# Kernel tuning notes

Hardware: AMD Instinct MI355X
Metric: run time of the kernel (lower is better)

## Reference

```python
import jax, jax.numpy as jnp
import numpy as np

B, S, LD, Hh, Ww = 64, 32, 16, 32, 18
D, NH, HD, FF, L = 512, 8, 64, 2048, 6
IN = LD * Hh * Ww  # 9216
EPS = 1e-5


def setup_inputs() -> dict:
    key = jax.random.key(0)
    ks = jax.random.split(key, 8)
    p = lambda k, s: jax.random.normal(k, s, jnp.float32) * 0.02
    return {
        "x": jax.random.normal(ks[0], (B, S, LD, Hh, Ww), jnp.float32),
        "inp_w": p(ks[1], (D, IN)), "inp_b": jnp.zeros((D,), jnp.float32),
        "in_proj_w": p(ks[2], (L, 3 * D, D)), "in_proj_b": jnp.zeros((L, 3 * D), jnp.float32),
        "out_w": p(ks[3], (L, D, D)), "out_b": jnp.zeros((L, D), jnp.float32),
        "ln1_w": jnp.ones((L, D), jnp.float32), "ln1_b": jnp.zeros((L, D), jnp.float32),
        "ln2_w": jnp.ones((L, D), jnp.float32), "ln2_b": jnp.zeros((L, D), jnp.float32),
        "ff1_w": p(ks[4], (L, FF, D)), "ff1_b": jnp.zeros((L, FF), jnp.float32),
        "ff2_w": p(ks[5], (L, D, FF)), "ff2_b": jnp.zeros((L, D), jnp.float32),
        "outp_w": p(ks[6], (IN, D)), "outp_b": jnp.zeros((IN,), jnp.float32),
    }


def _layernorm(x, w, b):
    mu = jnp.mean(x, -1, keepdims=True)
    var = jnp.mean(jnp.square(x - mu), -1, keepdims=True)
    return (x - mu) * jax.lax.rsqrt(var + EPS) * w + b


def _rope(x, cos, sin):
    # x: [B,S,NH,HD]; torchtune interleaved-pair rotation, rope applied BEFORE qk projection
    x2 = x.reshape(*x.shape[:-1], HD // 2, 2)
    x0, x1 = x2[..., 0], x2[..., 1]
    c = cos[None, :, None, :]
    s = sin[None, :, None, :]
    out = jnp.stack([x0 * c - x1 * s, x1 * c + x0 * s], axis=-1)
    return out.reshape(x.shape)


def reference(x, inp_w, inp_b, in_proj_w, in_proj_b, out_w, out_b,
              ln1_w, ln1_b, ln2_w, ln2_b, ff1_w, ff1_b, ff2_w, ff2_b,
              outp_w, outp_b):
    b, s = x.shape[0], x.shape[1]
    h = x.reshape(b, s, IN) @ inp_w.T + inp_b  # [B,S,D]

    theta = 1.0 / (10000.0 ** (jnp.arange(0, HD, 2, dtype=jnp.float32) / HD))
    ang = jnp.arange(s, dtype=jnp.float32)[:, None] * theta  # [S, HD/2]
    cos, sin = jnp.cos(ang), jnp.sin(ang)
    mask = jnp.triu(jnp.full((s, s), -jnp.inf, jnp.float32), k=1)  # causal additive mask
    scale = 1.0 / np.sqrt(HD)

    for i in range(L):
        # RoPE on full hidden state (pre-projection), used for q and k; v uses unrotated h
        hr = _rope(h.reshape(b, s, NH, HD), cos, sin).reshape(b, s, D)
        wq, wk, wv = in_proj_w[i, :D], in_proj_w[i, D:2 * D], in_proj_w[i, 2 * D:]
        bq, bk, bv = in_proj_b[i, :D], in_proj_b[i, D:2 * D], in_proj_b[i, 2 * D:]
        q = (hr @ wq.T + bq).reshape(b, s, NH, HD)
        k = (hr @ wk.T + bk).reshape(b, s, NH, HD)
        v = (h @ wv.T + bv).reshape(b, s, NH, HD)
        scores = jnp.einsum('bqhd,bkhd->bhqk', q, k) * scale + mask
        attn = jax.nn.softmax(scores, axis=-1)
        ctx = jnp.einsum('bhqk,bkhd->bqhd', attn, v).reshape(b, s, D)
        sa = ctx @ out_w[i].T + out_b[i]
        h = _layernorm(h + sa, ln1_w[i], ln1_b[i])  # post-norm (norm_first=False)
        ff = jax.nn.gelu(h @ ff1_w[i].T + ff1_b[i], approximate=False) @ ff2_w[i].T + ff2_b[i]
        h = _layernorm(h + ff, ln2_w[i], ln2_b[i])

    out = h @ outp_w.T + outp_b
    return out.reshape(b, s, LD, Hh, Ww)
```

## Files before the change

kernel.cpp:

```cpp
#include <hip/hip_runtime.h>
#include <hip/hip_bf16.h>
#include <math.h>


typedef __attribute__((ext_vector_type(8))) short bf16x8;
typedef __attribute__((ext_vector_type(4))) short bf16x4;
typedef __attribute__((ext_vector_type(8))) float f32x8;
typedef __attribute__((ext_vector_type(4))) float f32x4;

#define LN_EPS 1e-5f

__device__ inline float bf2f(__hip_bfloat16 v) { return __bfloat162float(v); }
__device__ inline __hip_bfloat16 f2bf(float f) { return __float2bfloat16(f); }

__device__ __forceinline__ void gload_lds16(const __hip_bfloat16* g, __hip_bfloat16* l) {
    __builtin_amdgcn_global_load_lds(
        (const __attribute__((address_space(1))) unsigned*)g,
        (__attribute__((address_space(3))) unsigned*)l, 16, 0, 0);
}

__device__ __forceinline__ void sync_tile() {
    asm volatile("s_waitcnt vmcnt(0) lgkmcnt(0)" ::: "memory");
    __builtin_amdgcn_s_barrier();
    asm volatile("" ::: "memory");
}

__global__ __launch_bounds__(1024) void rope_prep(float* __restrict__ tab) {
    const int t = threadIdx.x;
    const int s = t >> 5, p = t & 31;
    const float theta = powf(10000.f, -(float)p / 32.f);
    float sn, cs;
    sincosf((float)s * theta, &sn, &cs);
    tab[t * 2] = cs;
    tab[t * 2 + 1] = sn;
}

struct CvtSeg { const float* src; __hip_bfloat16* dst; };
struct CvtArgs { CvtSeg seg[16]; long cum[17]; };

__global__ __launch_bounds__(256) void convert_all(CvtArgs a, long total8) {
    for (long i = (long)blockIdx.x * 256 + threadIdx.x; i < total8;
         i += (long)gridDim.x * 256) {
        int s = 0;
        while (i >= a.cum[s + 1]) ++s;
        const long off = i - a.cum[s];
        const f32x8 x = *((const f32x8*)a.seg[s].src + off);
        union { bf16x8 v; __hip_bfloat16 b[8]; } o;
#pragma unroll
        for (int t = 0; t < 8; ++t) o.b[t] = f2bf(x[t]);
        *((bf16x8*)a.seg[s].dst + off) = o.v;
    }
}

template<int BM, int BN, int EPI, int OUT, int AMODE, int SWZ>
__global__ __launch_bounds__(256) void gemm_bt(
    const void* __restrict__ Araw, int bn_split,
    const float* __restrict__ rtab,
    const __hip_bfloat16* __restrict__ W,
    const __hip_bfloat16* __restrict__ bias,
    void* __restrict__ Cv,
    int M, int N, int Ktot, int KC)
{
    constexpr int FM = BM / 32, FN = BN / 32;
    constexpr int CPT_A = BM / 32, CPT_B = BN / 32;
    __shared__ __align__(16) __hip_bfloat16 sA[BM * 64];
    __shared__ __align__(16) __hip_bfloat16 sB[BN * 64];

    const int tid = threadIdx.x, lane = tid & 63, wave = tid >> 6;
    const int wr = wave >> 1, wc = wave & 1;
    const int lr = lane & 15, lk = lane >> 4;

    int bm, bn, zz;
    if (SWZ == 0) {
        const int nbm = gridDim.x, nbn = gridDim.y;
        const int nwg = nbm * nbn;
        const int orig = blockIdx.y * nbm + blockIdx.x;
        const int q8 = nwg >> 3, r8 = nwg & 7;
        const int xcd = orig & 7, loc = orig >> 3;
        const int f = (xcd < r8 ? xcd * (q8 + 1) : r8 * (q8 + 1) + (xcd - r8) * q8) + loc;
        bm = f % nbm; bn = f / nbm; zz = blockIdx.z;
    } else {
        const int bid = blockIdx.x;
        const int xcd = bid & 7, loc = bid >> 3;
        const int nbn = N / BN;
        const int per = (gridDim.x >> 3) / nbn;
        bn = loc % nbn;
        const int gid = xcd * per + loc / nbn;
        bm = gid % (M / BM); zz = gid / (M / BM);
    }
    const int kbeg = zz * KC, kend = kbeg + KC;
    const bool dorot = (AMODE == 2) && (bn < bn_split);

    const __hip_bfloat16* Ab = (const __hip_bfloat16*)Araw + (long)bm * BM * Ktot;
    const float*          Af = (const float*)Araw + (long)bm * BM * Ktot;
    const __hip_bfloat16* Wb = W + (long)bn * BN * Ktot;

    f32x4 acc[FM][FN];
#pragma unroll
    for (int i = 0; i < FM; ++i)
#pragma unroll
        for (int j = 0; j < FN; ++j) acc[i][j] = (f32x4){0.f, 0.f, 0.f, 0.f};

    f32x8  aregf[CPT_A];
    bf16x8 aregb[CPT_A];
    f32x8  csreg[CPT_A];

    auto stageA_g = [&](int k0) {
#pragma unroll
        for (int c = 0; c < CPT_A; ++c) {
            const int ch = tid + c * 256, row = ch >> 3, co = ch & 7;
            gload_lds16(&Ab[(long)row * Ktot + k0 + ((co ^ (row & 7)) * 8)],
                        (__hip_bfloat16*)((char*)sA + ch * 16));
        }
    };
    auto stageB_g = [&](int k0) {
#pragma unroll
        for (int c = 0; c < CPT_B; ++c) {
            const int ch = tid + c * 256, row = ch >> 3, co = ch & 7;
            gload_lds16(&Wb[(long)row * Ktot + k0 + ((co ^ (row & 7)) * 8)],
                        (__hip_bfloat16*)((char*)sB + ch * 16));
        }
    };
    auto issueA = [&](int k0) {
#pragma unroll
        for (int c = 0; c < CPT_A; ++c) {
            const int ch = tid + c * 256, row = ch >> 3, co = ch & 7;
            if (AMODE == 1) aregf[c] = *(const f32x8*)&Af[(long)row * Ktot + k0 + co * 8];
            if (AMODE == 2) {
                aregb[c] = *(const bf16x8*)&Ab[(long)row * Ktot + k0 + co * 8];
                if (dorot)
                    csreg[c] = *(const f32x8*)&rtab[((bm * BM + row) & 31) * 64 + co * 8];
            }
        }
    };
    auto writeA = [&]() {
#pragma unroll
        for (int c = 0; c < CPT_A; ++c) {
            const int ch = tid + c * 256, row = ch >> 3, co = ch & 7;
            union { bf16x8 v; __hip_bfloat16 b[8]; } t;
            if (AMODE == 1) {
#pragma unroll
                for (int j = 0; j < 8; ++j) t.b[j] = f2bf(aregf[c][j]);
            } else {
                t.v = aregb[c];
                if (dorot) {
#pragma unroll
                    for (int qd = 0; qd < 4; ++qd) {
                        const float c_ = csreg[c][qd * 2], sn = csreg[c][qd * 2 + 1];
                        const float x0 = bf2f(t.b[2 * qd]);
                        const float x1 = bf2f(t.b[2 * qd + 1]);
                        t.b[2 * qd]     = f2bf(x0 * c_ - x1 * sn);
                        t.b[2 * qd + 1] = f2bf(x1 * c_ + x0 * sn);
                    }
                }
            }
            *(bf16x8*)((char*)sA + row * 128 + ((co ^ (row & 7)) << 4)) = t.v;
        }
    };
    auto compute = [&]() {
        bf16x8 af[2][FM], bfr[2][FN];
#pragma unroll
        for (int ks = 0; ks < 2; ++ks) {
#pragma unroll
            for (int i = 0; i < FM; ++i) {
                const int row = wr * (BM / 2) + i * 16 + lr;
                const int co = ks * 4 + lk;
                af[ks][i] = *(const bf16x8*)((const char*)sA + row * 128 +
                                             ((co ^ (row & 7)) << 4));
            }
#pragma unroll
            for (int j = 0; j < FN; ++j) {
                const int row = wc * (BN / 2) + j * 16 + lr;
                const int co = ks * 4 + lk;
                bfr[ks][j] = *(const bf16x8*)((const char*)sB + row * 128 +
                                              ((co ^ (row & 7)) << 4));
            }
        }
#pragma unroll
        for (int ks = 0; ks < 2; ++ks)
#pragma unroll
            for (int i = 0; i < FM; ++i)
#pragma unroll
                for (int j = 0; j < FN; ++j)
                    acc[i][j] = __builtin_amdgcn_mfma_f32_16x16x32_bf16(
                        af[ks][i], bfr[ks][j], acc[i][j], 0, 0, 0);
    };

    if (AMODE != 0) issueA(kbeg);
    for (int k0 = kbeg; k0 < kend; k0 += 64) {
        if (k0 > kbeg) __builtin_amdgcn_s_barrier();
        if (AMODE == 0) stageA_g(k0);
        stageB_g(k0);
        if (AMODE != 0) writeA();
        sync_tile();
        if (AMODE != 0 && k0 + 64 < kend) issueA(k0 + 64);
        compute();
    }

    const int row0 = bm * BM + wr * (BM / 2);
    const int col0 = bn * BN + wc * (BN / 2);
    if (OUT == 1) {
        float* Cp = (float*)Cv + (long)zz * M * N;
#pragma unroll
        for (int i = 0; i < FM; ++i)
#pragma unroll
            for (int j = 0; j < FN; ++j) {
                const int col = col0 + j * 16 + lr;
#pragma unroll
                for (int r = 0; r < 4; ++r)
                    Cp[(long)(row0 + i * 16 + lk * 4 + r) * N + col] = acc[i][j][r];
            }
    } else {
#pragma unroll
        for (int i = 0; i < FM; ++i)
#pragma unroll
            for (int j = 0; j < FN; ++j) {
                const int col = col0 + j * 16 + lr;
                const float bv = bf2f(bias[col]);
#pragma unroll
                for (int r = 0; r < 4; ++r) {
                    const int row = row0 + i * 16 + lk * 4 + r;
                    float v = acc[i][j][r] + bv;
                    if (EPI == 1) v = 0.5f * v * (1.0f + erff(v * 0.70710678118654752f));
                    const long idx = (long)row * N + col;
                    if (OUT == 2) ((float*)Cv)[idx] = v;
                    else          ((__hip_bfloat16*)Cv)[idx] = f2bf(v);
                }
            }
    }
}

template<int SK>
__global__ __launch_bounds__(256) void sk_reduce(
    const float* __restrict__ part, const __hip_bfloat16* __restrict__ bias,
    __hip_bfloat16* __restrict__ out)
{
    const long MN = 2048L * 512;
    const long i4 = ((long)blockIdx.x * 256 + threadIdx.x) * 4;
    f32x4 s = (f32x4){0.f, 0.f, 0.f, 0.f};
#pragma unroll
    for (int z = 0; z < SK; ++z) s += *(const f32x4*)&part[z * MN + i4];
    const int col = (int)(i4 & 511);
    union { bf16x4 v; __hip_bfloat16 b[4]; } o;
#pragma unroll
    for (int j = 0; j < 4; ++j) o.b[j] = f2bf(s[j] + bf2f(bias[col + j]));
    *(bf16x4*)&out[i4] = o.v;
}

__global__ __launch_bounds__(256) void attn_mfma(
    const __hip_bfloat16* __restrict__ qkv, __hip_bfloat16* __restrict__ ctx)
{
    __shared__ __align__(16) __hip_bfloat16 sP[4][32 * 32];
    __shared__ __align__(16) __hip_bfloat16 sVT[4][64 * 32];

    const int wave = threadIdx.x >> 6, lane = threadIdx.x & 63;
    const int bh = blockIdx.x * 4 + wave;
    const int b = bh >> 3, head = bh & 7;
    const long tok0 = (long)b * 32;
    const int lr = lane & 15, lk = lane >> 4;

    const __hip_bfloat16* Qb = qkv + tok0 * 1536 + head * 64;
    const __hip_bfloat16* Kb = Qb + 512;
    const __hip_bfloat16* Vb = Qb + 1024;

#pragma unroll
    for (int t = 0; t < 4; ++t) {
        const int c = lane + t * 64, row = c >> 3, d0 = (c & 7) * 8;
        union { bf16x8 v; __hip_bfloat16 e[8]; } u;
        u.v = *(const bf16x8*)&Vb[(long)row * 1536 + d0];
#pragma unroll
        for (int e = 0; e < 8; ++e) sVT[wave][(d0 + e) * 32 + row] = u.e[e];
    }

    f32x4 sc[2][2];
#pragma unroll
    for (int i = 0; i < 2; ++i)
#pragma unroll
        for (int j = 0; j < 2; ++j) sc[i][j] = (f32x4){0.f, 0.f, 0.f, 0.f};
#pragma unroll
    for (int ks = 0; ks < 2; ++ks) {
        bf16x8 aq[2], bk[2];
#pragma unroll
        for (int i = 0; i < 2; ++i)
            aq[i] = *(const bf16x8*)&Qb[(long)(i * 16 + lr) * 1536 + ks * 32 + lk * 8];
#pragma unroll
        for (int j = 0; j < 2; ++j)
            bk[j] = *(const bf16x8*)&Kb[(long)(j * 16 + lr) * 1536 + ks * 32 + lk * 8];
#pragma unroll
        for (int i = 0; i < 2; ++i)
#pragma unroll
            for (int j = 0; j < 2; ++j)
                sc[i][j] = __builtin_amdgcn_mfma_f32_16x16x32_bf16(aq[i], bk[j], sc[i][j], 0, 0, 0);
    }

    float p[2][2][4], inv[2][4];
#pragma unroll
    for (int i = 0; i < 2; ++i) {
#pragma unroll
        for (int r = 0; r < 4; ++r) {
            const int row = i * 16 + lk * 4 + r;
            float m = -3.0e38f;
#pragma unroll
            for (int j = 0; j < 2; ++j) {
                const int col = j * 16 + lr;
                const float v = (col <= row) ? sc[i][j][r] * 0.125f : -3.0e38f;
                p[i][j][r] = v;
                m = fmaxf(m, v);
            }
#pragma unroll
            for (int off = 1; off < 16; off <<= 1)
                m = fmaxf(m, __shfl_xor(m, off));
            float l = 0.f;
#pragma unroll
            for (int j = 0; j < 2; ++j) {
                p[i][j][r] = expf(p[i][j][r] - m);
                l += p[i][j][r];
            }
#pragma unroll
            for (int off = 1; off < 16; off <<= 1)
                l += __shfl_xor(l, off);
            inv[i][r] = 1.f / l;
        }
    }

#pragma unroll
    for (int i = 0; i < 2; ++i)
#pragma unroll
        for (int j = 0; j < 2; ++j)
#pragma unroll
            for (int r = 0; r < 4; ++r)
                sP[wave][(i * 16 + lk * 4 + r) * 32 + j * 16 + lr] = f2bf(p[i][j][r]);

    bf16x8 pa[2], vb[4];
#pragma unroll
    for (int i = 0; i < 2; ++i)
        pa[i] = *(const bf16x8*)&sP[wave][(i * 16 + lr) * 32 + lk * 8];
#pragma unroll
    for (int j = 0; j < 4; ++j)
        vb[j] = *(const bf16x8*)&sVT[wave][(j * 16 + lr) * 32 + lk * 8];

    f32x4 o[2][4];
#pragma unroll
    for (int i = 0; i < 2; ++i)
#pragma unroll
        for (int j = 0; j < 4; ++j) {
            o[i][j] = (f32x4){0.f, 0.f, 0.f, 0.f};
            o[i][j] = __builtin_amdgcn_mfma_f32_16x16x32_bf16(pa[i], vb[j], o[i][j], 0, 0, 0);
        }

#pragma unroll
    for (int i = 0; i < 2; ++i)
#pragma unroll
        for (int j = 0; j < 4; ++j) {
            const int col = j * 16 + lr;
#pragma unroll
            for (int r = 0; r < 4; ++r) {
                const int row = i * 16 + lk * 4 + r;
                ctx[(tok0 + row) * 512 + head * 64 + col] = f2bf(o[i][j][r] * inv[i][r]);
            }
        }
}

__global__ __launch_bounds__(256) void add_ln_kernel(
    const __hip_bfloat16* __restrict__ a, const __hip_bfloat16* __restrict__ d,
    const __hip_bfloat16* __restrict__ w, const __hip_bfloat16* __restrict__ bias,
    __hip_bfloat16* __restrict__ out)
{
    const int wave = threadIdx.x >> 6, lane = threadIdx.x & 63;
    const long row = (long)blockIdx.x * 4 + wave;
    const long base = row * 512 + lane * 8;

    union { bf16x8 v; __hip_bfloat16 b[8]; } ua, ud, uo;
    ua.v = *(const bf16x8*)&a[base];
    ud.v = *(const bf16x8*)&d[base];

    float x[8];
    float s = 0.f, s2 = 0.f;
#pragma unroll
    for (int j = 0; j < 8; ++j) {
        x[j] = bf2f(ua.b[j]) + bf2f(ud.b[j]);
        s += x[j];
        s2 += x[j] * x[j];
    }
#pragma unroll
    for (int off = 32; off; off >>= 1) {
        s  += __shfl_xor(s, off);
        s2 += __shfl_xor(s2, off);
    }
    const float mu = s * (1.f / 512.f);
    const float var = s2 * (1.f / 512.f) - mu * mu;
    const float rs = rsqrtf(var + LN_EPS);
#pragma unroll
    for (int j = 0; j < 8; ++j) {
        const int col = lane * 8 + j;
        uo.b[j] = f2bf((x[j] - mu) * rs * bf2f(w[col]) + bf2f(bias[col]));
    }
    *(bf16x8*)&out[base] = uo.v;
}

extern "C" void kernel_launch(void* const* d_in, const int* in_sizes, int n_in,
                              void* d_out, int out_size, void* d_ws, size_t ws_size,
                              hipStream_t stream)
{
    const int M = 2048;
    __hip_bfloat16* wts = (__hip_bfloat16*)d_ws;

    const long O_INPW   = 0;
    const long O_INPROJ = 4718592;
    const long O_OUTW   = 9437184;
    const long O_FF1    = 11010048;
    const long O_FF2    = 17301504;
    const long O_OUTPW  = 23592960;
    const long O_INPB   = 28311552;
    const long O_INPROJB= 28312064;
    const long O_OUTB   = 28321280;
    const long O_LN1W   = 28324352;
    const long O_LN1B   = 28327424;
    const long O_LN2W   = 28330496;
    const long O_LN2B   = 28333568;
    const long O_FF1B   = 28336640;
    const long O_FF2B   = 28348928;
    const long O_OUTPB  = 28352000;
    const long O_ACT    = 28361216;

    __hip_bfloat16* h   = wts + O_ACT;
    __hip_bfloat16* ht  = h   + (long)M * 512;
    __hip_bfloat16* qkv = ht  + (long)M * 512;
    __hip_bfloat16* ctx = qkv + (long)M * 1536;
    __hip_bfloat16* sa  = ctx + (long)M * 512;
    __hip_bfloat16* ffh = sa  + (long)M * 512;
    __hip_bfloat16* ffo = ffh + (long)M * 2048;
    float* rtab = (float*)(ffo + (long)M * 512);
    float* skpart = (float*)((__hip_bfloat16*)rtab + 8192);

    rope_prep<<<1, 1024, 0, stream>>>(rtab);

    const int  cidx[16] = {1, 3, 5, 11, 13, 15, 2, 4, 6, 7, 8, 9, 10, 12, 14, 16};
    const long coff[16] = {O_INPW, O_INPROJ, O_OUTW, O_FF1, O_FF2, O_OUTPW,
                           O_INPB, O_INPROJB, O_OUTB, O_LN1W, O_LN1B, O_LN2W,
                           O_LN2B, O_FF1B, O_FF2B, O_OUTPB};
    const long csz[16]  = {4718592, 4718592, 1572864, 6291456, 6291456, 4718592,
                           512, 9216, 3072, 3072, 3072, 3072, 3072, 12288, 3072, 9216};
    CvtArgs ca;
    long cum = 0;
    for (int s = 0; s < 16; ++s) {
        ca.seg[s].src = (const float*)d_in[cidx[s]];
        ca.seg[s].dst = wts + coff[s];
        ca.cum[s] = cum;
        cum += csz[s] / 8;
    }
    ca.cum[16] = cum;
    convert_all<<<2048, 256, 0, stream>>>(ca, cum);

    gemm_bt<128, 128, 0, 1, 1, 1><<<512, 256, 0, stream>>>(
        d_in[0], 0, rtab, wts + O_INPW, wts + O_INPB, skpart, M, 512, 9216, 1152);
    sk_reduce<8><<<1024, 256, 0, stream>>>(skpart, wts + O_INPB, h);

    for (int i = 0; i < 6; ++i) {
        const __hip_bfloat16* wqkv = wts + O_INPROJ + (long)i * 1536 * 512;
        const __hip_bfloat16* bqkv = wts + O_INPROJB + i * 1536;

        gemm_bt<64, 64, 0, 0, 2, 0><<<dim3(32, 24), 256, 0, stream>>>(
            h, 16, rtab, wqkv, bqkv, qkv, M, 1536, 512, 512);
        attn_mfma<<<128, 256, 0, stream>>>(qkv, ctx);
        gemm_bt<64, 64, 0, 0, 0, 0><<<dim3(32, 8), 256, 0, stream>>>(
            ctx, 0, rtab, wts + O_OUTW + (long)i * 512 * 512, wts + O_OUTB + i * 512,
            sa, M, 512, 512, 512);
        add_ln_kernel<<<512, 256, 0, stream>>>(
            h, sa, wts + O_LN1W + i * 512, wts + O_LN1B + i * 512, ht);
        gemm_bt<64, 64, 1, 0, 0, 0><<<dim3(32, 32), 256, 0, stream>>>(
            ht, 0, rtab, wts + O_FF1 + (long)i * 2048 * 512, wts + O_FF1B + i * 2048,
            ffh, M, 2048, 512, 512);
        gemm_bt<64, 64, 0, 0, 0, 0><<<dim3(32, 8), 256, 0, stream>>>(
            ffh, 0, rtab, wts + O_FF2 + (long)i * 512 * 2048, wts + O_FF2B + i * 512,
            ffo, M, 512, 2048, 2048);
        add_ln_kernel<<<512, 256, 0, stream>>>(
            ht, ffo, wts + O_LN2W + i * 512, wts + O_LN2B + i * 512, h);
    }

    gemm_bt<128, 128, 0, 2, 0, 0><<<dim3(16, 72), 256, 0, stream>>>(
        h, 0, rtab, wts + O_OUTPW, wts + O_OUTPB, d_out, M, 9216, 512, 512);
}
```

Baseline: 543.5 us.

## Split-K the out-proj and FF2 GEMMs and fuse reduction into add+LayerNorm

The out-projection and FF2 GEMMs (N=512, only 256 tiles) now use split-K (2 and 4 ways) writing fp32 partials. A new kernel sums the partials, adds bias and residual, and applies LayerNorm in one pass, replacing the separate add_ln kernels and the sa/ffo buffers. The input projection's split factor rises from 8 to 16 when the workspace allows. This adds occupancy on narrow GEMMs at the cost of extra fp32 partial traffic through memory.

```diff
diff --git a/kernel.cpp b/kernel.cpp
--- a/kernel.cpp
+++ b/kernel.cpp
@@ -230,21 +230,63 @@
     }
 }
 
-template<int SK>
-__global__ __launch_bounds__(256) void sk_reduce(
+__global__ __launch_bounds__(256) void sk_reduce_rt(
     const float* __restrict__ part, const __hip_bfloat16* __restrict__ bias,
-    __hip_bfloat16* __restrict__ out)
+    __hip_bfloat16* __restrict__ out, int SK)
 {
     const long MN = 2048L * 512;
     const long i4 = ((long)blockIdx.x * 256 + threadIdx.x) * 4;
     f32x4 s = (f32x4){0.f, 0.f, 0.f, 0.f};
-#pragma unroll
     for (int z = 0; z < SK; ++z) s += *(const f32x4*)&part[z * MN + i4];
     const int col = (int)(i4 & 511);
     union { bf16x4 v; __hip_bfloat16 b[4]; } o;
 #pragma unroll
     for (int j = 0; j < 4; ++j) o.b[j] = f2bf(s[j] + bf2f(bias[col + j]));
     *(bf16x4*)&out[i4] = o.v;
+}
+
+template<int SK>
+__global__ __launch_bounds__(256) void skred_add_ln(
+    const float* __restrict__ part, const __hip_bfloat16* __restrict__ bias,
+    const __hip_bfloat16* __restrict__ resid,
+    const __hip_bfloat16* __restrict__ w, const __hip_bfloat16* __restrict__ b,
+    __hip_bfloat16* __restrict__ out)
+{
+    const long MN = 2048L * 512;
+    const int wave = threadIdx.x >> 6, lane = threadIdx.x & 63;
+    const long row = (long)blockIdx.x * 4 + wave;
+    const long base = row * 512 + lane * 8;
+
+    f32x8 acc = *(const f32x8*)&part[base];
+#pragma unroll
+    for (int z = 1; z < SK; ++z) acc += *(const f32x8*)&part[z * MN + base];
+
+    union { bf16x8 v; __hip_bfloat16 b[8]; } ur, uo;
+    ur.v = *(const bf16x8*)&resid[base];
+
+    float x[8];
+    float s = 0.f, s2 = 0.f;
+#pragma unroll
+    for (int j = 0; j < 8; ++j) {
+        const int col = lane * 8 + j;
+        x[j] = acc[j] + bf2f(bias[col]) + bf2f(ur.b[j]);
+        s += x[j];
+        s2 += x[j] * x[j];
+    }
+#pragma unroll
+    for (int off = 32; off; off >>= 1) {
+        s  += __shfl_xor(s, off);
+        s2 += __shfl_xor(s2, off);
+    }
+    const float mu = s * (1.f / 512.f);
+    const float var = s2 * (1.f / 512.f) - mu * mu;
+    const float rs = rsqrtf(var + LN_EPS);
+#pragma unroll
+    for (int j = 0; j < 8; ++j) {
+        const int col = lane * 8 + j;
+        uo.b[j] = f2bf((x[j] - mu) * rs * bf2f(w[col]) + bf2f(b[col]));
+    }
+    *(bf16x8*)&out[base] = uo.v;
 }
 
 __global__ __launch_bounds__(256) void attn_mfma(
@@ -359,43 +401,6 @@
                 ctx[(tok0 + row) * 512 + head * 64 + col] = f2bf(o[i][j][r] * inv[i][r]);
             }
         }
-}
-
-__global__ __launch_bounds__(256) void add_ln_kernel(
-    const __hip_bfloat16* __restrict__ a, const __hip_bfloat16* __restrict__ d,
-    const __hip_bfloat16* __restrict__ w, const __hip_bfloat16* __restrict__ bias,
-    __hip_bfloat16* __restrict__ out)
-{
-    const int wave = threadIdx.x >> 6, lane = threadIdx.x & 63;
-    const long row = (long)blockIdx.x * 4 + wave;
-    const long base = row * 512 + lane * 8;
-
-    union { bf16x8 v; __hip_bfloat16 b[8]; } ua, ud, uo;
-    ua.v = *(const bf16x8*)&a[base];
-    ud.v = *(const bf16x8*)&d[base];
-
-    float x[8];
-    float s = 0.f, s2 = 0.f;
-#pragma unroll
-    for (int j = 0; j < 8; ++j) {
-        x[j] = bf2f(ua.b[j]) + bf2f(ud.b[j]);
-        s += x[j];
-        s2 += x[j] * x[j];
-    }
-#pragma unroll
-    for (int off = 32; off; off >>= 1) {
-        s  += __shfl_xor(s, off);
-        s2 += __shfl_xor(s2, off);
-    }
-    const float mu = s * (1.f / 512.f);
-    const float var = s2 * (1.f / 512.f) - mu * mu;
-    const float rs = rsqrtf(var + LN_EPS);
-#pragma unroll
-    for (int j = 0; j < 8; ++j) {
-        const int col = lane * 8 + j;
-        uo.b[j] = f2bf((x[j] - mu) * rs * bf2f(w[col]) + bf2f(bias[col]));
-    }
-    *(bf16x8*)&out[base] = uo.v;
 }
 
 extern "C" void kernel_launch(void* const* d_in, const int* in_sizes, int n_in,
@@ -427,11 +432,12 @@
     __hip_bfloat16* ht  = h   + (long)M * 512;
     __hip_bfloat16* qkv = ht  + (long)M * 512;
     __hip_bfloat16* ctx = qkv + (long)M * 1536;
-    __hip_bfloat16* sa  = ctx + (long)M * 512;
-    __hip_bfloat16* ffh = sa  + (long)M * 512;
-    __hip_bfloat16* ffo = ffh + (long)M * 2048;
-    float* rtab = (float*)(ffo + (long)M * 512);
-    float* skpart = (float*)((__hip_bfloat16*)rtab + 8192);
+    __hip_bfloat16* ffh = ctx + (long)M * 512;
+    float* rtab = (float*)(ffh + (long)M * 2048);
+    float* skpart = (float*)((__hip_bfloat16*)rtab + 4096);
+
+    const long skpart_byte_off = (char*)skpart - (char*)d_ws;
+    const int zin = (ws_size >= (size_t)skpart_byte_off + 16L * M * 512 * 4) ? 16 : 8;
 
     rope_prep<<<1, 1024, 0, stream>>>(rtab);
 
@@ -452,9 +458,9 @@
     ca.cum[16] = cum;
     convert_all<<<2048, 256, 0, stream>>>(ca, cum);
 
-    gemm_bt<128, 128, 0, 1, 1, 1><<<512, 256, 0, stream>>>(
-        d_in[0], 0, rtab, wts + O_INPW, wts + O_INPB, skpart, M, 512, 9216, 1152);
-    sk_reduce<8><<<1024, 256, 0, stream>>>(skpart, wts + O_INPB, h);
+    gemm_bt<128, 128, 0, 1, 1, 1><<<64 * zin, 256, 0, stream>>>(
+        d_in[0], 0, rtab, wts + O_INPW, wts + O_INPB, skpart, M, 512, 9216, 9216 / zin);
+    sk_reduce_rt<<<1024, 256, 0, stream>>>(skpart, wts + O_INPB, h, zin);
 
     for (int i = 0; i < 6; ++i) {
         const __hip_bfloat16* wqkv = wts + O_INPROJ + (long)i * 1536 * 512;
@@ -463,19 +469,21 @@
         gemm_bt<64, 64, 0, 0, 2, 0><<<dim3(32, 24), 256, 0, stream>>>(
             h, 16, rtab, wqkv, bqkv, qkv, M, 1536, 512, 512);
         attn_mfma<<<128, 256, 0, stream>>>(qkv, ctx);
-        gemm_bt<64, 64, 0, 0, 0, 0><<<dim3(32, 8), 256, 0, stream>>>(
+        gemm_bt<64, 64, 0, 1, 0, 0><<<dim3(32, 8, 2), 256, 0, stream>>>(
             ctx, 0, rtab, wts + O_OUTW + (long)i * 512 * 512, wts + O_OUTB + i * 512,
-            sa, M, 512, 512, 512);
-        add_ln_kernel<<<512, 256, 0, stream>>>(
-            h, sa, wts + O_LN1W + i * 512, wts + O_LN1B + i * 512, ht);
+            skpart, M, 512, 512, 256);
+        skred_add_ln<2><<<512, 256, 0, stream>>>(
+            skpart, wts + O_OUTB + i * 512, h,
+            wts + O_LN1W + i * 512, wts + O_LN1B + i * 512, ht);
         gemm_bt<64, 64, 1, 0, 0, 0><<<dim3(32, 32), 256, 0, stream>>>(
             ht, 0, rtab, wts + O_FF1 + (long)i * 2048 * 512, wts + O_FF1B + i * 2048,
             ffh, M, 2048, 512, 512);
-        gemm_bt<64, 64, 0, 0, 0, 0><<<dim3(32, 8), 256, 0, stream>>>(
+        gemm_bt<64, 64, 0, 1, 0, 0><<<dim3(32, 8, 4), 256, 0, stream>>>(
             ffh, 0, rtab, wts + O_FF2 + (long)i * 512 * 2048, wts + O_FF2B + i * 512,
-            ffo, M, 512, 2048, 2048);
-        add_ln_kernel<<<512, 256, 0, stream>>>(
-            ht, ffo, wts + O_LN2W + i * 512, wts + O_LN2B + i * 512, h);
+            skpart, M, 512, 2048, 512);
+        skred_add_ln<4><<<512, 256, 0, stream>>>(
+            skpart, wts + O_FF2B + i * 512, ht,
+            wts + O_LN2W + i * 512, wts + O_LN2B + i * 512, h);
     }
 
     gemm_bt<128, 128, 0, 2, 0, 0><<<dim3(16, 72), 256, 0, stream>>>(
```

After: 524.9 us. -3.4%, faster.
